# Kernel tuning notes

Hardware: AMD Instinct MI355X
Metric: run time of the kernel (lower is better)

Reference implementation:

```python
import jax, jax.numpy as jnp
import numpy as np

E, T_MAX, H, L, V = 384, 256, 6, 6, 65
DH = E // H  # 64
EPS = 1e-5


def setup_inputs() -> dict:
    key = jax.random.key(0)
    ks = jax.random.split(key, 24)
    B, T = 128, 256
    s = 0.02
    inp = {
        "input_indices": jax.random.randint(ks[0], (B, T), 0, V, dtype=jnp.int64) if jax.config.read("jax_enable_x64") else jax.random.randint(ks[0], (B, T), 0, V, dtype=jnp.int32),
        "targets": jax.random.randint(ks[1], (B, T), 0, V, dtype=jnp.int32),
        "tok_emb": s * jax.random.normal(ks[2], (V, E), jnp.float32),
        "pos_emb": s * jax.random.normal(ks[3], (T_MAX, E), jnp.float32),
        "Wq": s * jax.random.normal(ks[4], (L, H, E, DH), jnp.float32),
        "Wk": s * jax.random.normal(ks[5], (L, H, E, DH), jnp.float32),
        "Wv": s * jax.random.normal(ks[6], (L, H, E, DH), jnp.float32),
        "Wo": s * jax.random.normal(ks[7], (L, E, E), jnp.float32),
        "bo": jnp.zeros((L, E), jnp.float32),
        "ln1_s": jnp.ones((L, E), jnp.float32),
        "ln1_b": jnp.zeros((L, E), jnp.float32),
        "ln2_s": jnp.ones((L, E), jnp.float32),
        "ln2_b": jnp.zeros((L, E), jnp.float32),
        "W1": s * jax.random.normal(ks[8], (L, E, 4 * E), jnp.float32),
        "b1": jnp.zeros((L, 4 * E), jnp.float32),
        "W2": s * jax.random.normal(ks[9], (L, 4 * E, E), jnp.float32),
        "b2": jnp.zeros((L, E), jnp.float32),
        "lnf_s": jnp.ones((E,), jnp.float32),
        "lnf_b": jnp.zeros((E,), jnp.float32),
        "Wout": s * jax.random.normal(ks[10], (E, V), jnp.float32),
        "bout": jnp.zeros((V,), jnp.float32),
    }
    return inp


def _ln(x, s, b):
    m = x.mean(-1, keepdims=True)
    v = ((x - m) ** 2).mean(-1, keepdims=True)
    return (x - m) * jax.lax.rsqrt(v + EPS) * s + b


def _forward(input_indices, targets, tok_emb, pos_emb, Wq, Wk, Wv, Wo, bo,
             ln1_s, ln1_b, ln2_s, ln2_b, W1, b1, W2, b2, lnf_s, lnf_b, Wout, bout):
    B, T = input_indices.shape
    x = tok_emb[input_indices] + pos_emb[:T]  # [B,T,E]
    causal = jnp.tril(jnp.ones((T, T), bool))
    scale = DH ** -0.5

    def block(x, p):
        wq, wk, wv, wo, bo_, l1s, l1b, l2s, l2b, w1, b1_, w2, b2_ = p
        h = _ln(x, l1s, l1b)
        q = jnp.einsum("bte,hed->bhtd", h, wq)
        k = jnp.einsum("bte,hed->bhtd", h, wk)
        v = jnp.einsum("bte,hed->bhtd", h, wv)
        scores = jnp.einsum("bhtd,bhsd->bhts", q, k) * scale
        scores = jnp.where(causal, scores, -jnp.inf)
        w = jax.nn.softmax(scores, axis=-1)
        att = jnp.einsum("bhts,bhsd->bhtd", w, v)  # [B,H,T,DH]
        att = att.transpose(0, 2, 1, 3).reshape(B, T, E)  # concat heads
        x = x + att @ wo + bo_
        h2 = _ln(x, l2s, l2b)
        ff = jax.nn.relu(h2 @ w1 + b1_) @ w2 + b2_
        return x + ff, None

    x, _ = jax.lax.scan(block, x, (Wq, Wk, Wv, Wo, bo, ln1_s, ln1_b, ln2_s, ln2_b, W1, b1, W2, b2))
    x = _ln(x, lnf_s, lnf_b)
    logits = x @ Wout + bout  # [B,T,V]
    logp = jax.nn.log_softmax(logits, axis=-1)
    nll = -jnp.take_along_axis(logp, targets[..., None], axis=-1)[..., 0]
    loss = nll.mean()
    return logits, loss


def reference(input_indices, targets, tok_emb, pos_emb, Wq, Wk, Wv, Wo, bo,
              ln1_s, ln1_b, ln2_s, ln2_b, W1, b1, W2, b2, lnf_s, lnf_b, Wout, bout):
    return _forward(input_indices, targets, tok_emb, pos_emb, Wq, Wk, Wv, Wo, bo,
                    ln1_s, ln1_b, ln2_s, ln2_b, W1, b1, W2, b2, lnf_s, lnf_b, Wout, bout)
```

## Files before the change

### kernel.cpp

```cpp
#include <hip/hip_runtime.h>

#define BT      32768
#define T_SEQ   256
#define E_DIM   384
#define NH      6
#define NL      6
#define VOC     65
#define FF_DIM  1536
#define QKV_N   1152

typedef short bf16x8 __attribute__((ext_vector_type(8)));
typedef float f32x4  __attribute__((ext_vector_type(4)));
typedef unsigned short u16;

typedef const unsigned int __attribute__((address_space(1))) gu32;
typedef unsigned int       __attribute__((address_space(3))) lu32;

__device__ __forceinline__ u16 f2bf(float x) {
  unsigned u = __builtin_bit_cast(unsigned, x);
  u += 0x7fffu + ((u >> 16) & 1u);
  return (u16)(u >> 16);
}
__device__ __forceinline__ float bf2f(u16 v) {
  unsigned u = ((unsigned)v) << 16;
  return __builtin_bit_cast(float, u);
}

__device__ __forceinline__ void load_lds_16(const void* g, void* l) {
  __builtin_amdgcn_global_load_lds((gu32*)g, (lu32*)l, 16, 0, 0);
}

__global__ __launch_bounds__(256) void transpose_t(
    const float* __restrict__ src, u16* __restrict__ dst, int R, int C,
    long sbs, long dbs_outer, int inner, long dbs_inner, long dbase) {
  __shared__ float t[32][33];
  const int b = blockIdx.z;
  const float* s = src + (long)b * sbs;
  u16* d = dst + dbase + (long)(b / inner) * dbs_outer + (long)(b % inner) * dbs_inner;
  const int r0 = blockIdx.x * 32, c0 = blockIdx.y * 32;
  const int tx = threadIdx.x & 31, ty = threadIdx.x >> 5;
#pragma unroll
  for (int i = 0; i < 4; i++) {
    int rr = ty + i * 8;
    int r = r0 + rr, c = c0 + tx;
    if (r < R && c < C) t[rr][tx] = s[(long)r * C + c];
  }
  __syncthreads();
#pragma unroll
  for (int i = 0; i < 4; i++) {
    int cc = ty + i * 8;
    int c = c0 + cc, r = r0 + tx;
    if (c < C && r < R) d[(long)c * R + r] = f2bf(t[tx][cc]);
  }
}

__global__ __launch_bounds__(256) void embed_k(const int* __restrict__ idx,
                                               const float* __restrict__ tok,
                                               const float* __restrict__ pos,
                                               u16* __restrict__ x) {
  int i = blockIdx.x * 256 + threadIdx.x;
  int bt = i / 48, q = i - bt * 48;
  int t = bt & 255;
  const float4* tp = (const float4*)(tok + (size_t)idx[bt] * E_DIM + q * 8);
  const float4* pp = (const float4*)(pos + (size_t)t * E_DIM + q * 8);
  float4 a0 = tp[0], a1 = tp[1], p0 = pp[0], p1 = pp[1];
  u16 o[8];
  o[0] = f2bf(a0.x + p0.x); o[1] = f2bf(a0.y + p0.y);
  o[2] = f2bf(a0.z + p0.z); o[3] = f2bf(a0.w + p0.w);
  o[4] = f2bf(a1.x + p1.x); o[5] = f2bf(a1.y + p1.y);
  o[6] = f2bf(a1.z + p1.z); o[7] = f2bf(a1.w + p1.w);
  *(bf16x8*)(x + (size_t)bt * E_DIM + q * 8) = *(bf16x8*)o;
}

__global__ __launch_bounds__(256) void ln_k(const u16* __restrict__ x,
                                            const float* __restrict__ gam,
                                            const float* __restrict__ bet,
                                            u16* __restrict__ out) {
  int tid = threadIdx.x, lane = tid & 63, w = tid >> 6;
  size_t token = (size_t)blockIdx.x * 4 + w;
  const u16* xr = x + token * E_DIM;
  u16 raw[6];
  *(uint2*)raw          = *(const uint2*)(xr + 4 * lane);
  *(unsigned*)(raw + 4) = *(const unsigned*)(xr + 256 + 2 * lane);
  float v[6]; float s = 0.f;
#pragma unroll
  for (int i = 0; i < 6; i++) { v[i] = bf2f(raw[i]); s += v[i]; }
#pragma unroll
  for (int d = 1; d < 64; d <<= 1) s += __shfl_xor(s, d);
  float mean = s * (1.f / E_DIM);
  float q = 0.f;
#pragma unroll
  for (int i = 0; i < 6; i++) { float d0 = v[i] - mean; q += d0 * d0; }
#pragma unroll
  for (int d = 1; d < 64; d <<= 1) q += __shfl_xor(q, d);
  float r = rsqrtf(q * (1.f / E_DIM) + 1e-5f);
  int e[6] = {4 * lane, 4 * lane + 1, 4 * lane + 2, 4 * lane + 3,
              256 + 2 * lane, 256 + 2 * lane + 1};
  u16 o[6];
#pragma unroll
  for (int i = 0; i < 6; i++)
    o[i] = f2bf((v[i] - mean) * r * gam[e[i]] + bet[e[i]]);
  u16* orow = out + token * E_DIM;
  *(uint2*)(orow + 4 * lane)        = *(uint2*)o;
  *(unsigned*)(orow + 256 + 2 * lane) = *(unsigned*)(o + 4);
}

__global__ __launch_bounds__(256) void gemm_bt(
    const u16* __restrict__ A, const u16* __restrict__ Bt, int K, int Nstore,
    const float* __restrict__ bias, const u16* __restrict__ resid,
    u16* __restrict__ outH, float* __restrict__ outF, int relu) {
  __shared__ u16 smem[8192];
  u16* As = smem;
  u16* Bs = smem + 4096;
  const int tid = threadIdx.x, lane = tid & 63, wv = tid >> 6;
  const int quad = lane >> 4, l16 = lane & 15;
  const int m0 = blockIdx.x * 128, n0 = blockIdx.y * 128;
  const int wm = (wv & 1) * 64, wn = (wv >> 1) * 64;
  const int srow = lane >> 2, scol = (lane & 3) * 8;

  f32x4 acc[4][4];
#pragma unroll
  for (int i = 0; i < 4; i++)
#pragma unroll
    for (int j = 0; j < 4; j++) acc[i][j] = (f32x4){0.f, 0.f, 0.f, 0.f};

  for (int k0 = 0; k0 < K; k0 += 32) {
    __syncthreads();
#pragma unroll
    for (int j = 0; j < 2; j++) {
      int rid = wv * 2 + j;
      int r = rid * 16 + srow;
      load_lds_16(A  + (size_t)(m0 + r) * K + (k0 + scol), &As[rid * 512]);
      load_lds_16(Bt + (size_t)(n0 + r) * K + (k0 + scol), &Bs[rid * 512]);
    }
    __syncthreads();
    bf16x8 af[4], bfr[4];
#pragma unroll
    for (int i = 0; i < 4; i++) af[i]  = *(const bf16x8*)&As[(wm + i * 16 + l16) * 32 + quad * 8];
#pragma unroll
    for (int j = 0; j < 4; j++) bfr[j] = *(const bf16x8*)&Bs[(wn + j * 16 + l16) * 32 + quad * 8];
#pragma unroll
    for (int i = 0; i < 4; i++)
#pragma unroll
      for (int j = 0; j < 4; j++)
        acc[i][j] = __builtin_amdgcn_mfma_f32_16x16x32_bf16(af[i], bfr[j], acc[i][j], 0, 0, 0);
  }

  if (outH) {
#pragma unroll
    for (int p = 0; p < 4; p++) {
      __syncthreads();
      if ((wv >> 1) == (p >> 1)) {
#pragma unroll
        for (int jj = 0; jj < 2; jj++) {
          int j = (p & 1) * 2 + jj;
          int gn = n0 + wn + j * 16 + l16;
          float bv = bias ? bias[gn] : 0.f;
          int lcol = jj * 16 + l16;
#pragma unroll
          for (int i = 0; i < 4; i++)
#pragma unroll
            for (int r = 0; r < 4; r++) {
              float v = acc[i][j][r] + bv;
              if (relu) v = fmaxf(v, 0.f);
              smem[(wm + i * 16 + quad * 4 + r) * 36 + lcol] = f2bf(v);
            }
        }
      }
      __syncthreads();
      const int gc0 = n0 + p * 32;
#pragma unroll
      for (int s = 0; s < 4; s++) {
        int row = s * 32 + (tid >> 3);
        int seg = (tid & 7) * 4;
        u16 pk[4];
        *(uint2*)pk = *(const uint2*)&smem[row * 36 + seg];
        size_t o = (size_t)(m0 + row) * Nstore + gc0 + seg;
        if (resid) {
          u16 rv[4];
          *(uint2*)rv = *(const uint2*)&resid[o];
#pragma unroll
          for (int q2 = 0; q2 < 4; q2++) pk[q2] = f2bf(bf2f(pk[q2]) + bf2f(rv[q2]));
        }
        *(uint2*)&outH[o] = *(uint2*)pk;
      }
    }
  } else {
#pragma unroll
    for (int j = 0; j < 4; j++) {
      const int gn = n0 + wn + j * 16 + l16;
      if (gn < Nstore) {
        const float bv = bias ? bias[gn] : 0.f;
#pragma unroll
        for (int i = 0; i < 4; i++)
#pragma unroll
          for (int r = 0; r < 4; r++) {
            const int gm = m0 + wm + i * 16 + quad * 4 + r;
            outF[(size_t)gm * Nstore + gn] = acc[i][j][r] + bv;
          }
      }
    }
  }
}

__global__ __launch_bounds__(512) void attn_k(const u16* __restrict__ qkv,
                                              u16* __restrict__ att) {
  __shared__ u16 Kc[64 * 64];
  __shared__ u16 Vtc[64 * 64];
  __shared__ u16 Pl[8 * 32 * 64];
  const int b = blockIdx.x / NH, h = blockIdx.x % NH;
  const int tid = threadIdx.x, lane = tid & 63, w = tid >> 6;
  const int quad = lane >> 4, l16 = lane & 15;
  const int rowb = b * T_SEQ;

  bf16x8 qf[2][2];
#pragma unroll
  for (int mi = 0; mi < 2; mi++)
#pragma unroll
    for (int kk = 0; kk < 2; kk++)
      qf[mi][kk] = *(const bf16x8*)(qkv + (size_t)(rowb + w * 32 + mi * 16 + l16) * QKV_N +
                                    h * 64 + kk * 32 + quad * 8);

  f32x4 Oa[2][4];
  float mrun[2][4], lrun[2][4];
#pragma unroll
  for (int mi = 0; mi < 2; mi++) {
#pragma unroll
    for (int di = 0; di < 4; di++) Oa[mi][di] = (f32x4){0.f, 0.f, 0.f, 0.f};
#pragma unroll
    for (int r = 0; r < 4; r++) { mrun[mi][r] = -1e30f; lrun[mi][r] = 0.f; }
  }

  u16* Pw = &Pl[w * 2048];
  const int nch = (w >> 1) + 1;
  const int sr = tid >> 3, sseg = (tid & 7) * 8;

  for (int c = 0; c < 4; c++) {
    const int s0 = c * 64;
    __syncthreads();
    *(uint4*)&Kc[sr * 64 + sseg] =
        *(const uint4*)(qkv + (size_t)(rowb + s0 + sr) * QKV_N + 384 + h * 64 + sseg);
    {
      union { uint4 u; u16 us[8]; } tb;
      tb.u = *(const uint4*)(qkv + (size_t)(rowb + s0 + sr) * QKV_N + 768 + h * 64 + sseg);
#pragma unroll
      for (int j = 0; j < 8; j++) Vtc[(sseg + j) * 64 + sr] = tb.us[j];
    }
    __syncthreads();
    if (c >= nch) continue;

    f32x4 S[2][4];
    bf16x8 kf[4][2];
#pragma unroll
    for (int ni = 0; ni < 4; ni++)
#pragma unroll
      for (int kk = 0; kk < 2; kk++)
        kf[ni][kk] = *(const bf16x8*)&Kc[(ni * 16 + l16) * 64 + kk * 32 + quad * 8];
#pragma unroll
    for (int mi = 0; mi < 2; mi++)
#pragma unroll
      for (int ni = 0; ni < 4; ni++) {
        f32x4 z = (f32x4){0.f, 0.f, 0.f, 0.f};
        z = __builtin_amdgcn_mfma_f32_16x16x32_bf16(qf[mi][0], kf[ni][0], z, 0, 0, 0);
        S[mi][ni] = __builtin_amdgcn_mfma_f32_16x16x32_bf16(qf[mi][1], kf[ni][1], z, 0, 0, 0);
      }
    const bool diag = (c == nch - 1);
#pragma unroll
    for (int mi = 0; mi < 2; mi++)
#pragma unroll
      for (int ni = 0; ni < 4; ni++)
#pragma unroll
        for (int r = 0; r < 4; r++) {
          float xv = S[mi][ni][r] * 0.125f;
          if (diag) {
            int t = w * 32 + mi * 16 + quad * 4 + r;
            int s = s0 + ni * 16 + l16;
            if (s > t) xv = -1e30f;
          }
          S[mi][ni][r] = xv;
        }
#pragma unroll
    for (int mi = 0; mi < 2; mi++)
#pragma unroll
      for (int r = 0; r < 4; r++) {
        float mx = fmaxf(fmaxf(S[mi][0][r], S[mi][1][r]), fmaxf(S[mi][2][r], S[mi][3][r]));
        mx = fmaxf(mx, __shfl_xor(mx, 1));
        mx = fmaxf(mx, __shfl_xor(mx, 2));
        mx = fmaxf(mx, __shfl_xor(mx, 4));
        mx = fmaxf(mx, __shfl_xor(mx, 8));
        float mnew = fmaxf(mrun[mi][r], mx);
        float alpha = __expf(mrun[mi][r] - mnew);
        float ls = 0.f;
#pragma unroll
        for (int ni = 0; ni < 4; ni++) {
          float p = __expf(S[mi][ni][r] - mnew);
          S[mi][ni][r] = p; ls += p;
        }
        ls += __shfl_xor(ls, 1); ls += __shfl_xor(ls, 2);
        ls += __shfl_xor(ls, 4); ls += __shfl_xor(ls, 8);
        lrun[mi][r] = lrun[mi][r] * alpha + ls;
        mrun[mi][r] = mnew;
#pragma unroll
        for (int di = 0; di < 4; di++) Oa[mi][di][r] *= alpha;
      }
#pragma unroll
    for (int mi = 0; mi < 2; mi++)
#pragma unroll
      for (int ni = 0; ni < 4; ni++)
#pragma unroll
        for (int r = 0; r < 4; r++)
          Pw[(mi * 16 + quad * 4 + r) * 64 + ni * 16 + l16] = f2bf(S[mi][ni][r]);
    bf16x8 pf[2][2], vf[4][2];
#pragma unroll
    for (int mi = 0; mi < 2; mi++)
#pragma unroll
      for (int kk = 0; kk < 2; kk++)
        pf[mi][kk] = *(const bf16x8*)&Pw[(mi * 16 + l16) * 64 + kk * 32 + quad * 8];
#pragma unroll
    for (int di = 0; di < 4; di++)
#pragma unroll
      for (int kk = 0; kk < 2; kk++)
        vf[di][kk] = *(const bf16x8*)&Vtc[(di * 16 + l16) * 64 + kk * 32 + quad * 8];
#pragma unroll
    for (int mi = 0; mi < 2; mi++)
#pragma unroll
      for (int di = 0; di < 4; di++) {
        Oa[mi][di] = __builtin_amdgcn_mfma_f32_16x16x32_bf16(pf[mi][0], vf[di][0], Oa[mi][di], 0, 0, 0);
        Oa[mi][di] = __builtin_amdgcn_mfma_f32_16x16x32_bf16(pf[mi][1], vf[di][1], Oa[mi][di], 0, 0, 0);
      }
  }

#pragma unroll
  for (int mi = 0; mi < 2; mi++)
#pragma unroll
    for (int r = 0; r < 4; r++) {
      float inv = 1.f / lrun[mi][r];
      int t = w * 32 + mi * 16 + quad * 4 + r;
#pragma unroll
      for (int di = 0; di < 4; di++)
        att[(size_t)(rowb + t) * E_DIM + h * 64 + di * 16 + l16] = f2bf(Oa[mi][di][r] * inv);
    }
}

__global__ __launch_bounds__(256) void loss_k(const float* __restrict__ logits,
                                              const int* __restrict__ tgt,
                                              float* __restrict__ loss) {
  __shared__ float part[4];
  const int tid = threadIdx.x, lane = tid & 63, w = tid >> 6;
  const int wave_id = blockIdx.x * 4 + w;
  float acc = 0.f;
  for (int t = wave_id; t < BT; t += 2048) {
    const float* row = logits + (size_t)t * VOC;
    float a = row[lane];
    float b = (lane == 0) ? row[64] : -1e30f;
    float mx = fmaxf(a, b);
#pragma unroll
    for (int d = 1; d < 64; d <<= 1) mx = fmaxf(mx, __shfl_xor(mx, d));
    float sum = __expf(a - mx) + ((lane == 0) ? __expf(b - mx) : 0.f);
#pragma unroll
    for (int d = 1; d < 64; d <<= 1) sum += __shfl_xor(sum, d);
    if (lane == 0) acc += mx + __logf(sum) - row[tgt[t]];
  }
  if (lane == 0) part[w] = acc;
  __syncthreads();
  if (tid == 0)
    atomicAdd(loss, (part[0] + part[1] + part[2] + part[3]) * (1.f / (float)BT));
}

extern "C" void kernel_launch(void* const* d_in, const int* in_sizes, int n_in,
                              void* d_out, int out_size, void* d_ws, size_t ws_size,
                              hipStream_t stream) {
  (void)in_sizes; (void)n_in; (void)out_size; (void)ws_size;
  const int*   idx  = (const int*)d_in[0];
  const int*   tgt  = (const int*)d_in[1];
  const float* tok  = (const float*)d_in[2];
  const float* pos  = (const float*)d_in[3];
  const float* Wq   = (const float*)d_in[4];
  const float* Wk   = (const float*)d_in[5];
  const float* Wv   = (const float*)d_in[6];
  const float* Wo   = (const float*)d_in[7];
  const float* bo   = (const float*)d_in[8];
  const float* ln1s = (const float*)d_in[9];
  const float* ln1b = (const float*)d_in[10];
  const float* ln2s = (const float*)d_in[11];
  const float* ln2b = (const float*)d_in[12];
  const float* W1   = (const float*)d_in[13];
  const float* b1   = (const float*)d_in[14];
  const float* W2   = (const float*)d_in[15];
  const float* b2   = (const float*)d_in[16];
  const float* lnfs = (const float*)d_in[17];
  const float* lnfb = (const float*)d_in[18];
  const float* Wout = (const float*)d_in[19];
  const float* bout = (const float*)d_in[20];

  char* w = (char*)d_ws;
  u16* x      = (u16*)w;    w += (size_t)BT * E_DIM * 2;
  u16* hb     = (u16*)w;    w += (size_t)BT * E_DIM * 2;
  u16* attb   = (u16*)w;    w += (size_t)BT * E_DIM * 2;
  u16* big    = (u16*)w;    w += (size_t)BT * FF_DIM * 2;
  u16* Wqkv_t = (u16*)w;    w += (size_t)NL * QKV_N * E_DIM * 2;
  u16* Wo_t   = (u16*)w;    w += (size_t)NL * E_DIM * E_DIM * 2;
  u16* W1_t   = (u16*)w;    w += (size_t)NL * FF_DIM * E_DIM * 2;
  u16* W2_t   = (u16*)w;    w += (size_t)NL * E_DIM * FF_DIM * 2;
  u16* Wout_t = (u16*)w;    w += (size_t)128 * E_DIM * 2;
  u16* qkv = big;
  u16* ff  = big;

  float* logits = (float*)d_out;
  float* loss   = logits + (size_t)BT * VOC;

  hipMemsetAsync(Wout_t, 0, 128 * E_DIM * 2, stream);
  transpose_t<<<dim3(12, 2, 36), 256, 0, stream>>>(Wq, Wqkv_t, 384, 64,
      24576, 442368, 6, 24576, 0);
  transpose_t<<<dim3(12, 2, 36), 256, 0, stream>>>(Wk, Wqkv_t, 384, 64,
      24576, 442368, 6, 24576, (long)384 * 384);
  transpose_t<<<dim3(12, 2, 36), 256, 0, stream>>>(Wv, Wqkv_t, 384, 64,
      24576, 442368, 6, 24576, (long)768 * 384);
  transpose_t<<<dim3(12, 12, 6), 256, 0, stream>>>(Wo, Wo_t, 384, 384,
      147456, 147456, 1, 0, 0);
  transpose_t<<<dim3(12, 48, 6), 256, 0, stream>>>(W1, W1_t, 384, 1536,
      589824, 589824, 1, 0, 0);
  transpose_t<<<dim3(48, 12, 6), 256, 0, stream>>>(W2, W2_t, 1536, 384,
      589824, 589824, 1, 0, 0);
  transpose_t<<<dim3(12, 3, 1), 256, 0, stream>>>(Wout, Wout_t, 384, 65,
      0, 0, 1, 0, 0);

  embed_k<<<6144, 256, 0, stream>>>(idx, tok, pos, x);

  for (int l = 0; l < NL; l++) {
    ln_k<<<8192, 256, 0, stream>>>(x, ln1s + l * E_DIM, ln1b + l * E_DIM, hb);
    gemm_bt<<<dim3(256, 9), 256, 0, stream>>>(hb, Wqkv_t + (size_t)l * QKV_N * E_DIM,
                                              384, QKV_N, nullptr, nullptr, qkv, nullptr, 0);
    attn_k<<<768, 512, 0, stream>>>(qkv, attb);
    gemm_bt<<<dim3(256, 3), 256, 0, stream>>>(attb, Wo_t + (size_t)l * E_DIM * E_DIM,
                                              384, E_DIM, bo + l * E_DIM, x, x, nullptr, 0);
    ln_k<<<8192, 256, 0, stream>>>(x, ln2s + l * E_DIM, ln2b + l * E_DIM, hb);
    gemm_bt<<<dim3(256, 12), 256, 0, stream>>>(hb, W1_t + (size_t)l * FF_DIM * E_DIM,
                                               384, FF_DIM, b1 + l * FF_DIM, nullptr, ff, nullptr, 1);
    gemm_bt<<<dim3(256, 3), 256, 0, stream>>>(ff, W2_t + (size_t)l * E_DIM * FF_DIM,
                                              1536, E_DIM, b2 + l * E_DIM, x, x, nullptr, 0);
  }
  ln_k<<<8192, 256, 0, stream>>>(x, lnfs, lnfb, hb);
  gemm_bt<<<dim3(256, 1), 256, 0, stream>>>(hb, Wout_t, 384, VOC, bout, nullptr, nullptr, logits, 0);

  hipMemsetAsync(loss, 0, 4, stream);
  loss_k<<<512, 256, 0, stream>>>(logits, tgt, loss);
}
```

Baseline: 1.912 ms.

## Double-buffer GEMM LDS tiles and XOR-swizzle chunks to avoid bank conflicts

The GEMM kernel now keeps two LDS buffers, so the global-to-LDS load of the next K tile is issued before the MFMAs on the current tile, with one barrier per iteration instead of two. The 16-byte chunks inside each LDS row are XOR-swizzled by row, and the fragment reads use the matching swizzle to reduce LDS bank conflicts. LDS use doubles to 32KB per block, which may lower occupancy. An unused variable `rs` is added.

```diff
diff --git a/kernel.cpp b/kernel.cpp
--- a/kernel.cpp
+++ b/kernel.cpp
@@ -101,22 +101,25 @@
   for (int i = 0; i < 6; i++)
     o[i] = f2bf((v[i] - mean) * r * gam[e[i]] + bet[e[i]]);
   u16* orow = out + token * E_DIM;
-  *(uint2*)(orow + 4 * lane)        = *(uint2*)o;
+  *(uint2*)(orow + 4 * lane)          = *(uint2*)o;
   *(unsigned*)(orow + 256 + 2 * lane) = *(unsigned*)(o + 4);
 }
 
-__global__ __launch_bounds__(256) void gemm_bt(
+__global__ __launch_bounds__(256) void gemm_d(
     const u16* __restrict__ A, const u16* __restrict__ Bt, int K, int Nstore,
     const float* __restrict__ bias, const u16* __restrict__ resid,
     u16* __restrict__ outH, float* __restrict__ outF, int relu) {
-  __shared__ u16 smem[8192];
+  __shared__ u16 smem[16384];
   u16* As = smem;
-  u16* Bs = smem + 4096;
+  u16* Bs = smem + 8192;
   const int tid = threadIdx.x, lane = tid & 63, wv = tid >> 6;
   const int quad = lane >> 4, l16 = lane & 15;
   const int m0 = blockIdx.x * 128, n0 = blockIdx.y * 128;
   const int wm = (wv & 1) * 64, wn = (wv >> 1) * 64;
-  const int srow = lane >> 2, scol = (lane & 3) * 8;
+
+  const int lrow = lane >> 2;
+  const int lchunk = (lane & 3) ^ (lrow & 3);
+  const int rs = quad == 0 ? 0 : quad;
 
   f32x4 acc[4][4];
 #pragma unroll
@@ -124,32 +127,42 @@
 #pragma unroll
     for (int j = 0; j < 4; j++) acc[i][j] = (f32x4){0.f, 0.f, 0.f, 0.f};
 
-  for (int k0 = 0; k0 < K; k0 += 32) {
-    __syncthreads();
+  auto stage = [&](int sel, int k0) {
 #pragma unroll
     for (int j = 0; j < 2; j++) {
       int rid = wv * 2 + j;
-      int r = rid * 16 + srow;
-      load_lds_16(A  + (size_t)(m0 + r) * K + (k0 + scol), &As[rid * 512]);
-      load_lds_16(Bt + (size_t)(n0 + r) * K + (k0 + scol), &Bs[rid * 512]);
+      int r = rid * 16 + lrow;
+      load_lds_16(A + (size_t)(m0 + r) * K + k0 + lchunk * 8, &As[sel * 4096 + rid * 512]);
+      load_lds_16(Bt + (size_t)(n0 + r) * K + k0 + lchunk * 8, &Bs[sel * 4096 + rid * 512]);
     }
-    __syncthreads();
+  };
+
+  const int NK = K >> 5;
+  stage(0, 0);
+  __syncthreads();
+  for (int kt = 0; kt < NK; kt++) {
+    const int cur = kt & 1;
+    if (kt + 1 < NK) stage(cur ^ 1, (kt + 1) * 32);
+    const u16* Ab = As + cur * 4096;
+    const u16* Bb = Bs + cur * 4096;
+    const int slot = (quad ^ (l16 & 3)) * 8;
     bf16x8 af[4], bfr[4];
 #pragma unroll
-    for (int i = 0; i < 4; i++) af[i]  = *(const bf16x8*)&As[(wm + i * 16 + l16) * 32 + quad * 8];
-#pragma unroll
-    for (int j = 0; j < 4; j++) bfr[j] = *(const bf16x8*)&Bs[(wn + j * 16 + l16) * 32 + quad * 8];
+    for (int i = 0; i < 4; i++) af[i]  = *(const bf16x8*)&Ab[(wm + i * 16 + l16) * 32 + slot];
+#pragma unroll
+    for (int j = 0; j < 4; j++) bfr[j] = *(const bf16x8*)&Bb[(wn + j * 16 + l16) * 32 + slot];
 #pragma unroll
     for (int i = 0; i < 4; i++)
 #pragma unroll
       for (int j = 0; j < 4; j++)
         acc[i][j] = __builtin_amdgcn_mfma_f32_16x16x32_bf16(af[i], bfr[j], acc[i][j], 0, 0, 0);
+    __syncthreads();
   }
 
   if (outH) {
 #pragma unroll
     for (int p = 0; p < 4; p++) {
-      __syncthreads();
+      if (p) __syncthreads();
       if ((wv >> 1) == (p >> 1)) {
 #pragma unroll
         for (int jj = 0; jj < 2; jj++) {
@@ -429,19 +442,19 @@
 
   for (int l = 0; l < NL; l++) {
     ln_k<<<8192, 256, 0, stream>>>(x, ln1s + l * E_DIM, ln1b + l * E_DIM, hb);
-    gemm_bt<<<dim3(256, 9), 256, 0, stream>>>(hb, Wqkv_t + (size_t)l * QKV_N * E_DIM,
-                                              384, QKV_N, nullptr, nullptr, qkv, nullptr, 0);
+    gemm_d<<<dim3(256, 9), 256, 0, stream>>>(hb, Wqkv_t + (size_t)l * QKV_N * E_DIM,
+                                             384, QKV_N, nullptr, nullptr, qkv, nullptr, 0);
     attn_k<<<768, 512, 0, stream>>>(qkv, attb);
-    gemm_bt<<<dim3(256, 3), 256, 0, stream>>>(attb, Wo_t + (size_t)l * E_DIM * E_DIM,
-                                              384, E_DIM, bo + l * E_DIM, x, x, nullptr, 0);
+    gemm_d<<<dim3(256, 3), 256, 0, stream>>>(attb, Wo_t + (size_t)l * E_DIM * E_DIM,
+                                             384, E_DIM, bo + l * E_DIM, x, x, nullptr, 0);
     ln_k<<<8192, 256, 0, stream>>>(x, ln2s + l * E_DIM, ln2b + l * E_DIM, hb);
-    gemm_bt<<<dim3(256, 12), 256, 0, stream>>>(hb, W1_t + (size_t)l * FF_DIM * E_DIM,
-                                               384, FF_DIM, b1 + l * FF_DIM, nullptr, ff, nullptr, 1);
-    gemm_bt<<<dim3(256, 3), 256, 0, stream>>>(ff, W2_t + (size_t)l * E_DIM * FF_DIM,
-                                              1536, E_DIM, b2 + l * E_DIM, x, x, nullptr, 0);
+    gemm_d<<<dim3(256, 12), 256, 0, stream>>>(hb, W1_t + (size_t)l * FF_DIM * E_DIM,
+                                              384, FF_DIM, b1 + l * FF_DIM, nullptr, ff, nullptr, 1);
+    gemm_d<<<dim3(256, 3), 256, 0, stream>>>(ff, W2_t + (size_t)l * E_DIM * FF_DIM,
+                                             1536, E_DIM, b2 + l * E_DIM, x, x, nullptr, 0);
   }
   ln_k<<<8192, 256, 0, stream>>>(x, lnfs, lnfb, hb);
-  gemm_bt<<<dim3(256, 1), 256, 0, stream>>>(hb, Wout_t, 384, VOC, bout, nullptr, nullptr, logits, 0);
+  gemm_d<<<dim3(256, 1), 256, 0, stream>>>(hb, Wout_t, 384, VOC, bout, nullptr, nullptr, logits, 0);
 
   hipMemsetAsync(loss, 0, 4, stream);
   loss_k<<<512, 256, 0, stream>>>(logits, tgt, loss);
```

Result: faster. 1.801 ms (-5.8%).
